# Optimization experiments

Hardware: AMD Instinct MI355X
Metric: run time of the kernel (lower is better)

Reference implementation:

```python
import jax, jax.numpy as jnp
import numpy as np

EPS = 1e-5
GROUPS = 8

def _bn(x, g, b, axes):
    # training-mode batch norm over `axes`, channel axis = 1
    m = jnp.mean(x, axis=axes, keepdims=True)
    v = jnp.var(x, axis=axes, keepdims=True)
    shp = (1, -1) + (1,) * (x.ndim - 2)
    return (x - m) / jnp.sqrt(v + EPS) * g.reshape(shp) + b.reshape(shp)

def setup_inputs() -> dict:
    key = jax.random.key(0)
    k0, k1, k2 = jax.random.split(key, 3)
    N, C, T, V = 64, 256, 64, 25
    out_planes = 256
    gp = out_planes // GROUPS  # 32
    x = jax.random.normal(k0, (N, C, T, V), jnp.float32)
    w_qkv = jax.random.normal(k1, (2 * out_planes, C), jnp.float32) * np.float32(np.sqrt(1.0 / C))
    relative = jax.random.normal(k2, (2 * gp, 2 * V - 1), jnp.float32) * np.float32(np.sqrt(1.0 / gp))
    return {
        "x": x,
        "w_qkv": w_qkv,
        "relative": relative,
        "bn_qkv_g": jnp.ones(2 * out_planes, jnp.float32),
        "bn_qkv_b": jnp.zeros(2 * out_planes, jnp.float32),
        "bn_sim_g": jnp.ones(3 * GROUPS, jnp.float32),
        "bn_sim_b": jnp.zeros(3 * GROUPS, jnp.float32),
        "bn_out_g": jnp.ones(2 * out_planes, jnp.float32),
        "bn_out_b": jnp.zeros(2 * out_planes, jnp.float32),
    }

def reference(x, w_qkv, relative, bn_qkv_g, bn_qkv_b, bn_sim_g, bn_sim_b, bn_out_g, bn_out_b):
    N, C, T, V = x.shape
    out_planes = w_qkv.shape[0] // 2
    gp = out_planes // GROUPS
    K = V  # kernel_size == V by construction
    # static relative index table
    qi = np.arange(K)[None, :]
    ki = np.arange(K)[:, None]
    flat_idx = (ki - qi + K - 1).reshape(-1)
    # mean over frames T (permute(0,2,1,3) then mean over dim1 == mean over axis 2)
    y = jnp.mean(x, axis=2)  # [N, C, V]
    # 1x1 conv qkv + BN1d
    qkv = _bn(jnp.einsum('oc,ncv->nov', w_qkv, y), bn_qkv_g, bn_qkv_b, (0, 2))
    qkv = qkv.reshape(N, GROUPS, 2 * gp, V)
    q, k, v = qkv[:, :, : gp // 2], qkv[:, :, gp // 2: gp], qkv[:, :, gp:]
    all_emb = relative[:, flat_idx].reshape(2 * gp, K, K)
    q_e, k_e, v_e = all_emb[: gp // 2], all_emb[gp // 2: gp], all_emb[gp:]
    qr = jnp.einsum('ngci,cij->ngij', q, q_e)
    kr = jnp.einsum('ngci,cij->ngij', k, k_e).swapaxes(2, 3)
    qk = jnp.einsum('ngci,ngcj->ngij', q, k)
    stacked = jnp.concatenate([qk, qr, kr], axis=1)  # [N, 3*groups, V, V]
    stacked = _bn(stacked, bn_sim_g, bn_sim_b, (0, 2, 3)).reshape(N, 3, GROUPS, V, V).sum(axis=1)
    sim = jax.nn.softmax(stacked, axis=3)  # [N, groups, V, V]
    sv = jnp.einsum('ngij,ngcj->ngci', sim, v)
    sve = jnp.einsum('ngij,cij->ngci', sim, v_e)
    so = jnp.concatenate([sv, sve], axis=-1).reshape(N, 2 * out_planes, V)
    o = _bn(so, bn_out_g, bn_out_b, (0, 2)).reshape(N, out_planes, 2, V).sum(axis=2)
    o = jax.nn.sigmoid(o)[:, :, None, :]  # [N, out_planes, 1, V]
    return x + x * o
```

## Files before the change

### kernel.cpp

```cpp
#include <hip/hip_runtime.h>
#include <cmath>

#define NN 64
#define CC 256
#define TT 64
#define VV 25
#define OO 512
#define GG 8
#define NV (NN*VV)
#define STK 625

__global__ __launch_bounds__(256) void k_mean(const float* __restrict__ x,
                                              float* __restrict__ y) {
    __shared__ float tile[TT * VV];
    int b = blockIdx.x;
    const float4* x4 = (const float4*)(x + (size_t)b * (TT * VV));
    float4* t4 = (float4*)tile;
    for (int i = threadIdx.x; i < (TT * VV) / 4; i += 256) t4[i] = x4[i];
    __syncthreads();
    if (threadIdx.x < VV) {
        float s = 0.f;
        #pragma unroll
        for (int t = 0; t < TT; ++t) s += tile[t * VV + threadIdx.x];
        y[(size_t)b * VV + threadIdx.x] = s * (1.0f / TT);
    }
}

__global__ __launch_bounds__(256) void k_gemm(const float* __restrict__ y,
                                              const float* __restrict__ w,
                                              float* __restrict__ qkv) {
    __shared__ float ys[CC][VV + 1];
    int n = blockIdx.x >> 3, oc = blockIdx.x & 7;
    const float* yp = y + (size_t)n * CC * VV;
    for (int i = threadIdx.x; i < CC * VV; i += 256) ys[i / VV][i % VV] = yp[i];
    __syncthreads();
    int t = threadIdx.x;
    if (t >= 200) return;
    int v = t % VV, o0 = t / VV;
    int obase = oc * 64 + o0;
    float acc[8] = {0, 0, 0, 0, 0, 0, 0, 0};
    for (int c = 0; c < CC; c += 4) {
        float y0 = ys[c][v], y1 = ys[c + 1][v], y2 = ys[c + 2][v], y3 = ys[c + 3][v];
        #pragma unroll
        for (int u = 0; u < 8; ++u) {
            const float4 w4 = *(const float4*)&w[(size_t)(obase + u * 8) * CC + c];
            acc[u] += y0 * w4.x + y1 * w4.y + y2 * w4.z + y3 * w4.w;
        }
    }
    #pragma unroll
    for (int u = 0; u < 8; ++u)
        qkv[((size_t)n * OO + obase + u * 8) * VV + v] = acc[u];
}

__global__ __launch_bounds__(256) void k_stats_nv(const float* __restrict__ t,
                                                  const float* __restrict__ g,
                                                  const float* __restrict__ b,
                                                  float* __restrict__ scale,
                                                  float* __restrict__ shift) {
    int ch = blockIdx.x;
    float s = 0.f, s2 = 0.f;
    for (int i = threadIdx.x; i < NV; i += 256) {
        int n = i / VV, v = i - n * VV;
        float val = t[((size_t)n * OO + ch) * VV + v];
        s += val; s2 += val * val;
    }
    __shared__ float ra[256], rb[256];
    ra[threadIdx.x] = s; rb[threadIdx.x] = s2;
    __syncthreads();
    for (int off = 128; off > 0; off >>= 1) {
        if (threadIdx.x < off) {
            ra[threadIdx.x] += ra[threadIdx.x + off];
            rb[threadIdx.x] += rb[threadIdx.x + off];
        }
        __syncthreads();
    }
    if (threadIdx.x == 0) {
        float m = ra[0] * (1.0f / NV);
        float var = rb[0] * (1.0f / NV) - m * m;
        float sc = g[ch] * rsqrtf(var + 1e-5f);
        scale[ch] = sc;
        shift[ch] = b[ch] - m * sc;
    }
}

__global__ __launch_bounds__(256) void k_scores(const float* __restrict__ qkv,
                                                const float* __restrict__ rel,
                                                const float* __restrict__ qsc,
                                                const float* __restrict__ qsh,
                                                float* __restrict__ stk) {
    int n = blockIdx.x >> 3, gidx = blockIdx.x & 7;
    __shared__ float qs[16][VV], ks[16][VV], rs[32][49];
    int t = threadIdx.x;
    for (int i = t; i < 32 * VV; i += 256) {
        int c = i / VV, v = i - c * VV;
        int o = gidx * 64 + c;
        float val = qkv[((size_t)n * OO + o) * VV + v] * qsc[o] + qsh[o];
        if (c < 16) qs[c][v] = val; else ks[c - 16][v] = val;
    }
    for (int i = t; i < 32 * 49; i += 256) rs[i / 49][i % 49] = rel[i];
    __syncthreads();
    for (int ij = t; ij < STK; ij += 256) {
        int i = ij / VV, j = ij - (ij / VV) * VV;
        float aqk = 0.f, aqr = 0.f, akr = 0.f;
        #pragma unroll
        for (int c = 0; c < 16; ++c) {
            float qv = qs[c][i], kv = ks[c][j];
            aqk += qv * kv;
            aqr += qv * rs[c][i - j + 24];
            akr += kv * rs[16 + c][j - i + 24];
        }
        size_t base = (size_t)n * 24;
        stk[(base + gidx) * STK + ij]      = aqk;
        stk[(base + 8 + gidx) * STK + ij]  = aqr;
        stk[(base + 16 + gidx) * STK + ij] = akr;
    }
}

__global__ __launch_bounds__(256) void k_stats24_a(const float* __restrict__ stk,
                                                   float* __restrict__ part) {
    int ch = blockIdx.x >> 4, chunk = blockIdx.x & 15;
    float s = 0.f, s2 = 0.f;
    for (int i = threadIdx.x; i < 4 * STK; i += 256) {
        int n = chunk * 4 + i / STK, r = i - (i / STK) * STK;
        float v = stk[((size_t)n * 24 + ch) * STK + r];
        s += v; s2 += v * v;
    }
    __shared__ float ra[256], rb[256];
    ra[threadIdx.x] = s; rb[threadIdx.x] = s2;
    __syncthreads();
    for (int off = 128; off > 0; off >>= 1) {
        if (threadIdx.x < off) {
            ra[threadIdx.x] += ra[threadIdx.x + off];
            rb[threadIdx.x] += rb[threadIdx.x + off];
        }
        __syncthreads();
    }
    if (threadIdx.x == 0) {
        part[(ch * 16 + chunk) * 2]     = ra[0];
        part[(ch * 16 + chunk) * 2 + 1] = rb[0];
    }
}

__global__ __launch_bounds__(64) void k_stats24_b(const float* __restrict__ part,
                                                  const float* __restrict__ g,
                                                  const float* __restrict__ b,
                                                  float* __restrict__ scale,
                                                  float* __restrict__ shift) {
    int ch = threadIdx.x;
    if (ch < 24) {
        float s = 0.f, s2 = 0.f;
        for (int k = 0; k < 16; ++k) {
            s  += part[(ch * 16 + k) * 2];
            s2 += part[(ch * 16 + k) * 2 + 1];
        }
        float m = s * (1.0f / 40000.0f);
        float var = s2 * (1.0f / 40000.0f) - m * m;
        float sc = g[ch] * rsqrtf(var + 1e-5f);
        scale[ch] = sc;
        shift[ch] = b[ch] - m * sc;
    }
}

__global__ __launch_bounds__(256) void k_attnout(const float* __restrict__ stk,
                                                 const float* __restrict__ qkv,
                                                 const float* __restrict__ rel,
                                                 const float* __restrict__ qsc,
                                                 const float* __restrict__ qsh,
                                                 const float* __restrict__ ssc,
                                                 const float* __restrict__ ssh,
                                                 float* __restrict__ so) {
    int n = blockIdx.x >> 3, gidx = blockIdx.x & 7;
    __shared__ float S[STK];
    __shared__ float vs[32][VV];
    __shared__ float rs[32][49];
    int t = threadIdx.x;
    const size_t sb = (size_t)n * 24 * STK;
    float sc0 = ssc[gidx],      sh0 = ssh[gidx];
    float sc1 = ssc[8 + gidx],  sh1 = ssh[8 + gidx];
    float sc2 = ssc[16 + gidx], sh2 = ssh[16 + gidx];
    for (int ij = t; ij < STK; ij += 256) {
        float a = stk[sb + (size_t)gidx * STK + ij] * sc0 + sh0;
        a += stk[sb + (size_t)(8 + gidx) * STK + ij] * sc1 + sh1;
        a += stk[sb + (size_t)(16 + gidx) * STK + ij] * sc2 + sh2;
        S[ij] = a;
    }
    for (int i = t; i < 32 * VV; i += 256) {
        int c = i / VV, v = i - (i / VV) * VV;
        int o = gidx * 64 + 32 + c;
        vs[c][v] = qkv[((size_t)n * OO + o) * VV + v] * qsc[o] + qsh[o];
    }
    for (int i = t; i < 32 * 49; i += 256) rs[i / 49][i % 49] = rel[32 * 49 + i];
    __syncthreads();
    if (t < VV) {
        int i = t;
        float m = -1e30f;
        #pragma unroll
        for (int j = 0; j < VV; ++j) m = fmaxf(m, S[i * VV + j]);
        float sum = 0.f;
        float e[VV];
        #pragma unroll
        for (int j = 0; j < VV; ++j) { e[j] = expf(S[i * VV + j] - m); sum += e[j]; }
        float inv = 1.0f / sum;
        #pragma unroll
        for (int j = 0; j < VV; ++j) S[i * VV + j] = e[j] * inv;
    }
    __syncthreads();
    for (int idx = t; idx < 32 * VV; idx += 256) {
        int c = idx / VV, i = idx - (idx / VV) * VV;
        float sv = 0.f, sve = 0.f;
        #pragma unroll
        for (int j = 0; j < VV; ++j) {
            float p = S[i * VV + j];
            sv  += p * vs[c][j];
            sve += p * rs[c][i - j + 24];
        }
        size_t o = (size_t)(gidx * 32 + c) * 2;
        so[((size_t)n * OO + o) * VV + i]     = sv;
        so[((size_t)n * OO + o + 1) * VV + i] = sve;
    }
}

__global__ __launch_bounds__(256) void k_final(const float* __restrict__ x,
                                               const float* __restrict__ so,
                                               const float* __restrict__ osc,
                                               const float* __restrict__ osh,
                                               float* __restrict__ out) {
    int b = blockIdx.x;
    int n = b >> 8, p = b & 255;
    __shared__ float orow[VV];
    if (threadIdx.x < VV) {
        int v = threadIdx.x;
        int o0 = 2 * p, o1 = 2 * p + 1;
        float a  = so[((size_t)n * OO + o0) * VV + v] * osc[o0] + osh[o0];
        float c2 = so[((size_t)n * OO + o1) * VV + v] * osc[o1] + osh[o1];
        float z = a + c2;
        orow[v] = 1.0f + 1.0f / (1.0f + expf(-z));
    }
    __syncthreads();
    const float4* x4 = (const float4*)(x + (size_t)b * (TT * VV));
    float4* y4 = (float4*)(out + (size_t)b * (TT * VV));
    for (int wv = threadIdx.x; wv < (TT * VV) / 4; wv += 256) {
        float4 xv = x4[wv];
        int e = 4 * wv;
        int v0 = e % VV;
        float4 r;
        int v;
        v = v0;                      r.x = xv.x * orow[v];
        v = v0 + 1; if (v >= VV) v -= VV; r.y = xv.y * orow[v];
        v = v0 + 2; if (v >= VV) v -= VV; r.z = xv.z * orow[v];
        v = v0 + 3; if (v >= VV) v -= VV; r.w = xv.w * orow[v];
        y4[wv] = r;
    }
}

extern "C" void kernel_launch(void* const* d_in, const int* in_sizes, int n_in,
                              void* d_out, int out_size, void* d_ws, size_t ws_size,
                              hipStream_t stream) {
    (void)in_sizes; (void)n_in; (void)out_size; (void)ws_size;
    const float* x        = (const float*)d_in[0];
    const float* w_qkv    = (const float*)d_in[1];
    const float* relative = (const float*)d_in[2];
    const float* bn_qkv_g = (const float*)d_in[3];
    const float* bn_qkv_b = (const float*)d_in[4];
    const float* bn_sim_g = (const float*)d_in[5];
    const float* bn_sim_b = (const float*)d_in[6];
    const float* bn_out_g = (const float*)d_in[7];
    const float* bn_out_b = (const float*)d_in[8];
    float* out = (float*)d_out;

    float* ws = (float*)d_ws;
    float* w_y    = ws;
    float* w_qkvp = ws + 409600;
    float* w_stk  = ws + 1228800;
    float* w_so   = ws + 2188800;
    float* qsc    = ws + 3008000;
    float* qsh    = qsc + 512;
    float* ssc    = qsh + 512;
    float* ssh    = ssc + 24;
    float* osc    = ssh + 24;
    float* osh    = osc + 512;
    float* w_part = osh + 512;

    k_mean<<<NN * CC, 256, 0, stream>>>(x, w_y);
    k_gemm<<<NN * 8, 256, 0, stream>>>(w_y, w_qkv, w_qkvp);
    k_stats_nv<<<OO, 256, 0, stream>>>(w_qkvp, bn_qkv_g, bn_qkv_b, qsc, qsh);
    k_scores<<<NN * GG, 256, 0, stream>>>(w_qkvp, relative, qsc, qsh, w_stk);
    k_stats24_a<<<24 * 16, 256, 0, stream>>>(w_stk, w_part);
    k_stats24_b<<<1, 64, 0, stream>>>(w_part, bn_sim_g, bn_sim_b, ssc, ssh);
    k_attnout<<<NN * GG, 256, 0, stream>>>(w_stk, w_qkvp, relative, qsc, qsh, ssc, ssh, w_so);
    k_stats_nv<<<OO, 256, 0, stream>>>(w_so, bn_out_g, bn_out_b, osc, osh);
    k_final<<<NN * CC, 256, 0, stream>>>(x, w_so, osc, osh, out);
}
```

Before: 281.5 us.

## Fuse batch-norm statistics into producer kernels via atomic accumulation

The separate BN statistics kernels (two k_stats_nv launches, k_stats24_a/b) are removed. Per-channel sum and sum-of-squares are now accumulated with atomicAdd inside the gemm, scores and attnout kernels, and consumers compute scale and shift on the fly. A memset zeroes the stat buffers. k_mean also splits its T reduction across more threads. This cuts four launches and the re-reads of intermediates, at the cost of float atomics with nondeterministic summation order.

```diff
diff --git a/kernel.cpp b/kernel.cpp
--- a/kernel.cpp
+++ b/kernel.cpp
@@ -13,92 +13,101 @@
 __global__ __launch_bounds__(256) void k_mean(const float* __restrict__ x,
                                               float* __restrict__ y) {
     __shared__ float tile[TT * VV];
+    __shared__ float part[8 * VV];
     int b = blockIdx.x;
+    int t = threadIdx.x;
     const float4* x4 = (const float4*)(x + (size_t)b * (TT * VV));
     float4* t4 = (float4*)tile;
-    for (int i = threadIdx.x; i < (TT * VV) / 4; i += 256) t4[i] = x4[i];
-    __syncthreads();
-    if (threadIdx.x < VV) {
-        float s = 0.f;
-        #pragma unroll
-        for (int t = 0; t < TT; ++t) s += tile[t * VV + threadIdx.x];
-        y[(size_t)b * VV + threadIdx.x] = s * (1.0f / TT);
+    for (int i = t; i < (TT * VV) / 4; i += 256) t4[i] = x4[i];
+    __syncthreads();
+    if (t < 200) {
+        int v = t % VV, s = t / VV;
+        float a = 0.f;
+        #pragma unroll
+        for (int k = 0; k < 8; ++k) a += tile[(s * 8 + k) * VV + v];
+        part[s * VV + v] = a;
+    }
+    __syncthreads();
+    if (t < VV) {
+        float a = 0.f;
+        #pragma unroll
+        for (int s = 0; s < 8; ++s) a += part[s * VV + t];
+        y[(size_t)b * VV + t] = a * (1.0f / TT);
     }
 }
 
 __global__ __launch_bounds__(256) void k_gemm(const float* __restrict__ y,
                                               const float* __restrict__ w,
-                                              float* __restrict__ qkv) {
-    __shared__ float ys[CC][VV + 1];
+                                              float* __restrict__ qkv,
+                                              float* __restrict__ qstat) {
+    __shared__ float ys[CC * VV];
     int n = blockIdx.x >> 3, oc = blockIdx.x & 7;
+    int t = threadIdx.x;
     const float* yp = y + (size_t)n * CC * VV;
-    for (int i = threadIdx.x; i < CC * VV; i += 256) ys[i / VV][i % VV] = yp[i];
-    __syncthreads();
-    int t = threadIdx.x;
-    if (t >= 200) return;
+    for (int i = t; i < CC * VV; i += 256) ys[i] = yp[i];
+    __syncthreads();
     int v = t % VV, o0 = t / VV;
     int obase = oc * 64 + o0;
     float acc[8] = {0, 0, 0, 0, 0, 0, 0, 0};
-    for (int c = 0; c < CC; c += 4) {
-        float y0 = ys[c][v], y1 = ys[c + 1][v], y2 = ys[c + 2][v], y3 = ys[c + 3][v];
-        #pragma unroll
-        for (int u = 0; u < 8; ++u) {
-            const float4 w4 = *(const float4*)&w[(size_t)(obase + u * 8) * CC + c];
-            acc[u] += y0 * w4.x + y1 * w4.y + y2 * w4.z + y3 * w4.w;
+    if (t < 200) {
+        for (int c = 0; c < CC; c += 4) {
+            float y0 = ys[c * VV + v], y1 = ys[(c + 1) * VV + v];
+            float y2 = ys[(c + 2) * VV + v], y3 = ys[(c + 3) * VV + v];
+            #pragma unroll
+            for (int u = 0; u < 8; ++u) {
+                const float4 w4 = *(const float4*)&w[(size_t)(obase + u * 8) * CC + c];
+                acc[u] += y0 * w4.x + y1 * w4.y + y2 * w4.z + y3 * w4.w;
+            }
         }
-    }
-    #pragma unroll
-    for (int u = 0; u < 8; ++u)
-        qkv[((size_t)n * OO + obase + u * 8) * VV + v] = acc[u];
-}
-
-__global__ __launch_bounds__(256) void k_stats_nv(const float* __restrict__ t,
-                                                  const float* __restrict__ g,
-                                                  const float* __restrict__ b,
-                                                  float* __restrict__ scale,
-                                                  float* __restrict__ shift) {
-    int ch = blockIdx.x;
-    float s = 0.f, s2 = 0.f;
-    for (int i = threadIdx.x; i < NV; i += 256) {
-        int n = i / VV, v = i - n * VV;
-        float val = t[((size_t)n * OO + ch) * VV + v];
-        s += val; s2 += val * val;
-    }
-    __shared__ float ra[256], rb[256];
-    ra[threadIdx.x] = s; rb[threadIdx.x] = s2;
-    __syncthreads();
-    for (int off = 128; off > 0; off >>= 1) {
-        if (threadIdx.x < off) {
-            ra[threadIdx.x] += ra[threadIdx.x + off];
-            rb[threadIdx.x] += rb[threadIdx.x + off];
-        }
-        __syncthreads();
-    }
-    if (threadIdx.x == 0) {
-        float m = ra[0] * (1.0f / NV);
-        float var = rb[0] * (1.0f / NV) - m * m;
-        float sc = g[ch] * rsqrtf(var + 1e-5f);
-        scale[ch] = sc;
-        shift[ch] = b[ch] - m * sc;
+        #pragma unroll
+        for (int u = 0; u < 8; ++u)
+            qkv[((size_t)n * OO + obase + u * 8) * VV + v] = acc[u];
+    }
+    __syncthreads();
+    if (t < 200) {
+        #pragma unroll
+        for (int u = 0; u < 8; ++u) ys[(o0 + 8 * u) * VV + v] = acc[u];
+    }
+    __syncthreads();
+    if (t < 64) {
+        float s = 0.f, s2 = 0.f;
+        #pragma unroll
+        for (int k = 0; k < VV; ++k) { float w0 = ys[t * VV + k]; s += w0; s2 += w0 * w0; }
+        int ch = oc * 64 + t;
+        atomicAdd(&qstat[2 * ch], s);
+        atomicAdd(&qstat[2 * ch + 1], s2);
     }
 }
 
 __global__ __launch_bounds__(256) void k_scores(const float* __restrict__ qkv,
                                                 const float* __restrict__ rel,
-                                                const float* __restrict__ qsc,
-                                                const float* __restrict__ qsh,
-                                                float* __restrict__ stk) {
+                                                const float* __restrict__ qstat,
+                                                const float* __restrict__ gq,
+                                                const float* __restrict__ bq,
+                                                float* __restrict__ stk,
+                                                float* __restrict__ sstat) {
     int n = blockIdx.x >> 3, gidx = blockIdx.x & 7;
     __shared__ float qs[16][VV], ks[16][VV], rs[32][49];
-    int t = threadIdx.x;
+    __shared__ float qscl[32], qshl[32];
+    __shared__ float red0[256], red1[256], red2[256];
+    int t = threadIdx.x;
+    if (t < 32) {
+        int o = gidx * 64 + t;
+        float s = qstat[2 * o], s2 = qstat[2 * o + 1];
+        float m = s * (1.0f / NV), var = s2 * (1.0f / NV) - m * m;
+        float sc = gq[o] * rsqrtf(var + 1e-5f);
+        qscl[t] = sc; qshl[t] = bq[o] - m * sc;
+    }
+    __syncthreads();
     for (int i = t; i < 32 * VV; i += 256) {
         int c = i / VV, v = i - c * VV;
         int o = gidx * 64 + c;
-        float val = qkv[((size_t)n * OO + o) * VV + v] * qsc[o] + qsh[o];
+        float val = qkv[((size_t)n * OO + o) * VV + v] * qscl[c] + qshl[c];
         if (c < 16) qs[c][v] = val; else ks[c - 16][v] = val;
     }
     for (int i = t; i < 32 * 49; i += 256) rs[i / 49][i % 49] = rel[i];
     __syncthreads();
+    float sqk = 0.f, sqr = 0.f, skr = 0.f, sqk2 = 0.f, sqr2 = 0.f, skr2 = 0.f;
     for (int ij = t; ij < STK; ij += 256) {
         int i = ij / VV, j = ij - (ij / VV) * VV;
         float aqk = 0.f, aqr = 0.f, akr = 0.f;
@@ -113,81 +122,81 @@
         stk[(base + gidx) * STK + ij]      = aqk;
         stk[(base + 8 + gidx) * STK + ij]  = aqr;
         stk[(base + 16 + gidx) * STK + ij] = akr;
-    }
-}
-
-__global__ __launch_bounds__(256) void k_stats24_a(const float* __restrict__ stk,
-                                                   float* __restrict__ part) {
-    int ch = blockIdx.x >> 4, chunk = blockIdx.x & 15;
-    float s = 0.f, s2 = 0.f;
-    for (int i = threadIdx.x; i < 4 * STK; i += 256) {
-        int n = chunk * 4 + i / STK, r = i - (i / STK) * STK;
-        float v = stk[((size_t)n * 24 + ch) * STK + r];
-        s += v; s2 += v * v;
-    }
-    __shared__ float ra[256], rb[256];
-    ra[threadIdx.x] = s; rb[threadIdx.x] = s2;
+        sqk += aqk; sqk2 += aqk * aqk;
+        sqr += aqr; sqr2 += aqr * aqr;
+        skr += akr; skr2 += akr * akr;
+    }
+    red0[t] = sqk; red1[t] = sqr; red2[t] = skr;
     __syncthreads();
     for (int off = 128; off > 0; off >>= 1) {
-        if (threadIdx.x < off) {
-            ra[threadIdx.x] += ra[threadIdx.x + off];
-            rb[threadIdx.x] += rb[threadIdx.x + off];
-        }
+        if (t < off) { red0[t] += red0[t + off]; red1[t] += red1[t + off]; red2[t] += red2[t + off]; }
         __syncthreads();
     }
-    if (threadIdx.x == 0) {
-        part[(ch * 16 + chunk) * 2]     = ra[0];
-        part[(ch * 16 + chunk) * 2 + 1] = rb[0];
-    }
-}
-
-__global__ __launch_bounds__(64) void k_stats24_b(const float* __restrict__ part,
-                                                  const float* __restrict__ g,
-                                                  const float* __restrict__ b,
-                                                  float* __restrict__ scale,
-                                                  float* __restrict__ shift) {
-    int ch = threadIdx.x;
-    if (ch < 24) {
-        float s = 0.f, s2 = 0.f;
-        for (int k = 0; k < 16; ++k) {
-            s  += part[(ch * 16 + k) * 2];
-            s2 += part[(ch * 16 + k) * 2 + 1];
-        }
-        float m = s * (1.0f / 40000.0f);
-        float var = s2 * (1.0f / 40000.0f) - m * m;
-        float sc = g[ch] * rsqrtf(var + 1e-5f);
-        scale[ch] = sc;
-        shift[ch] = b[ch] - m * sc;
+    if (t == 0) {
+        atomicAdd(&sstat[2 * gidx], red0[0]);
+        atomicAdd(&sstat[2 * (8 + gidx)], red1[0]);
+        atomicAdd(&sstat[2 * (16 + gidx)], red2[0]);
+    }
+    __syncthreads();
+    red0[t] = sqk2; red1[t] = sqr2; red2[t] = skr2;
+    __syncthreads();
+    for (int off = 128; off > 0; off >>= 1) {
+        if (t < off) { red0[t] += red0[t + off]; red1[t] += red1[t + off]; red2[t] += red2[t + off]; }
+        __syncthreads();
+    }
+    if (t == 0) {
+        atomicAdd(&sstat[2 * gidx + 1], red0[0]);
+        atomicAdd(&sstat[2 * (8 + gidx) + 1], red1[0]);
+        atomicAdd(&sstat[2 * (16 + gidx) + 1], red2[0]);
     }
 }
 
 __global__ __launch_bounds__(256) void k_attnout(const float* __restrict__ stk,
                                                  const float* __restrict__ qkv,
                                                  const float* __restrict__ rel,
-                                                 const float* __restrict__ qsc,
-                                                 const float* __restrict__ qsh,
-                                                 const float* __restrict__ ssc,
-                                                 const float* __restrict__ ssh,
-                                                 float* __restrict__ so) {
+                                                 const float* __restrict__ qstat,
+                                                 const float* __restrict__ gq,
+                                                 const float* __restrict__ bq,
+                                                 const float* __restrict__ sstat,
+                                                 const float* __restrict__ gs,
+                                                 const float* __restrict__ bs,
+                                                 float* __restrict__ so,
+                                                 float* __restrict__ ostat) {
     int n = blockIdx.x >> 3, gidx = blockIdx.x & 7;
     __shared__ float S[STK];
     __shared__ float vs[32][VV];
     __shared__ float rs[32][49];
-    int t = threadIdx.x;
+    __shared__ float scratch[64 * VV];
+    __shared__ float sscl[3], sshl[3], vscl[32], vshl[32];
+    int t = threadIdx.x;
+    if (t < 3) {
+        int ch = 8 * t + gidx;
+        float s = sstat[2 * ch], s2 = sstat[2 * ch + 1];
+        const float inv = 1.0f / 40000.0f;
+        float m = s * inv, var = s2 * inv - m * m;
+        float sc = gs[ch] * rsqrtf(var + 1e-5f);
+        sscl[t] = sc; sshl[t] = bs[ch] - m * sc;
+    }
+    if (t >= 32 && t < 64) {
+        int c = t - 32;
+        int o = gidx * 64 + 32 + c;
+        float s = qstat[2 * o], s2 = qstat[2 * o + 1];
+        float m = s * (1.0f / NV), var = s2 * (1.0f / NV) - m * m;
+        float sc = gq[o] * rsqrtf(var + 1e-5f);
+        vscl[c] = sc; vshl[c] = bq[o] - m * sc;
+    }
+    __syncthreads();
     const size_t sb = (size_t)n * 24 * STK;
-    float sc0 = ssc[gidx],      sh0 = ssh[gidx];
-    float sc1 = ssc[8 + gidx],  sh1 = ssh[8 + gidx];
-    float sc2 = ssc[16 + gidx], sh2 = ssh[16 + gidx];
     for (int ij = t; ij < STK; ij += 256) {
-        float a = stk[sb + (size_t)gidx * STK + ij] * sc0 + sh0;
-        a += stk[sb + (size_t)(8 + gidx) * STK + ij] * sc1 + sh1;
-        a += stk[sb + (size_t)(16 + gidx) * STK + ij] * sc2 + sh2;
+        float a = stk[sb + (size_t)gidx * STK + ij] * sscl[0] + sshl[0];
+        a += stk[sb + (size_t)(8 + gidx) * STK + ij] * sscl[1] + sshl[1];
+        a += stk[sb + (size_t)(16 + gidx) * STK + ij] * sscl[2] + sshl[2];
         S[ij] = a;
     }
     for (int i = t; i < 32 * VV; i += 256) {
         int c = i / VV, v = i - (i / VV) * VV;
         int o = gidx * 64 + 32 + c;
-        vs[c][v] = qkv[((size_t)n * OO + o) * VV + v] * qsc[o] + qsh[o];
+        vs[c][v] = qkv[((size_t)n * OO + o) * VV + v] * vscl[c] + vshl[c];
     }
     for (int i = t; i < 32 * 49; i += 256) rs[i / 49][i % 49] = rel[32 * 49 + i];
     __syncthreads();
@@ -217,29 +226,49 @@
         size_t o = (size_t)(gidx * 32 + c) * 2;
         so[((size_t)n * OO + o) * VV + i]     = sv;
         so[((size_t)n * OO + o + 1) * VV + i] = sve;
+        scratch[(2 * c) * VV + i]     = sv;
+        scratch[(2 * c + 1) * VV + i] = sve;
+    }
+    __syncthreads();
+    if (t < 64) {
+        float s = 0.f, s2 = 0.f;
+        #pragma unroll
+        for (int k = 0; k < VV; ++k) { float w0 = scratch[t * VV + k]; s += w0; s2 += w0 * w0; }
+        int ch = gidx * 64 + t;
+        atomicAdd(&ostat[2 * ch], s);
+        atomicAdd(&ostat[2 * ch + 1], s2);
     }
 }
 
 __global__ __launch_bounds__(256) void k_final(const float* __restrict__ x,
                                                const float* __restrict__ so,
-                                               const float* __restrict__ osc,
-                                               const float* __restrict__ osh,
+                                               const float* __restrict__ ostat,
+                                               const float* __restrict__ go,
+                                               const float* __restrict__ bo,
                                                float* __restrict__ out) {
     int b = blockIdx.x;
     int n = b >> 8, p = b & 255;
-    __shared__ float orow[VV];
-    if (threadIdx.x < VV) {
-        int v = threadIdx.x;
+    int t = threadIdx.x;
+    __shared__ float osl[2], oshl[2], orow[VV];
+    if (t < 2) {
+        int ch = 2 * p + t;
+        float s = ostat[2 * ch], s2 = ostat[2 * ch + 1];
+        float m = s * (1.0f / NV), var = s2 * (1.0f / NV) - m * m;
+        float sc = go[ch] * rsqrtf(var + 1e-5f);
+        osl[t] = sc; oshl[t] = bo[ch] - m * sc;
+    }
+    __syncthreads();
+    if (t < VV) {
         int o0 = 2 * p, o1 = 2 * p + 1;
-        float a  = so[((size_t)n * OO + o0) * VV + v] * osc[o0] + osh[o0];
-        float c2 = so[((size_t)n * OO + o1) * VV + v] * osc[o1] + osh[o1];
+        float a  = so[((size_t)n * OO + o0) * VV + t] * osl[0] + oshl[0];
+        float c2 = so[((size_t)n * OO + o1) * VV + t] * osl[1] + oshl[1];
         float z = a + c2;
-        orow[v] = 1.0f + 1.0f / (1.0f + expf(-z));
+        orow[t] = 1.0f + 1.0f / (1.0f + expf(-z));
     }
     __syncthreads();
     const float4* x4 = (const float4*)(x + (size_t)b * (TT * VV));
     float4* y4 = (float4*)(out + (size_t)b * (TT * VV));
-    for (int wv = threadIdx.x; wv < (TT * VV) / 4; wv += 256) {
+    for (int wv = t; wv < (TT * VV) / 4; wv += 256) {
         float4 xv = x4[wv];
         int e = 4 * wv;
         int v0 = e % VV;
@@ -273,21 +302,15 @@
     float* w_qkvp = ws + 409600;
     float* w_stk  = ws + 1228800;
     float* w_so   = ws + 2188800;
-    float* qsc    = ws + 3008000;
-    float* qsh    = qsc + 512;
-    float* ssc    = qsh + 512;
-    float* ssh    = ssc + 24;
-    float* osc    = ssh + 24;
-    float* osh    = osc + 512;
-    float* w_part = osh + 512;
+    float* qstat  = ws + 3008000;
+    float* sstat  = qstat + 1024;
+    float* ostat  = sstat + 48;
+    hipMemsetAsync(qstat, 0, 2096 * sizeof(float), stream);
 
     k_mean<<<NN * CC, 256, 0, stream>>>(x, w_y);
-    k_gemm<<<NN * 8, 256, 0, stream>>>(w_y, w_qkv, w_qkvp);
-    k_stats_nv<<<OO, 256, 0, stream>>>(w_qkvp, bn_qkv_g, bn_qkv_b, qsc, qsh);
-    k_scores<<<NN * GG, 256, 0, stream>>>(w_qkvp, relative, qsc, qsh, w_stk);
-    k_stats24_a<<<24 * 16, 256, 0, stream>>>(w_stk, w_part);
-    k_stats24_b<<<1, 64, 0, stream>>>(w_part, bn_sim_g, bn_sim_b, ssc, ssh);
-    k_attnout<<<NN * GG, 256, 0, stream>>>(w_stk, w_qkvp, relative, qsc, qsh, ssc, ssh, w_so);
-    k_stats_nv<<<OO, 256, 0, stream>>>(w_so, bn_out_g, bn_out_b, osc, osh);
-    k_final<<<NN * CC, 256, 0, stream>>>(x, w_so, osc, osh, out);
-}
+    k_gemm<<<NN * 8, 256, 0, stream>>>(w_y, w_qkv, w_qkvp, qstat);
+    k_scores<<<NN * GG, 256, 0, stream>>>(w_qkvp, relative, qstat, bn_qkv_g, bn_qkv_b, w_stk, sstat);
+    k_attnout<<<NN * GG, 256, 0, stream>>>(w_stk, w_qkvp, relative, qstat, bn_qkv_g, bn_qkv_b,
+                                           sstat, bn_sim_g, bn_sim_b, w_so, ostat);
+    k_final<<<NN * CC, 256, 0, stream>>>(x, w_so, ostat, bn_out_g, bn_out_b, out);
+}
```

Result: slower. 294.6 us (+4.7%).
